# Kernel tuning notes

Measured on AMD Instinct MI355X. Metric: run time of the kernel, lower is better.

Reference implementation:

```python
import jax, jax.numpy as jnp
import numpy as np

EPS_KERAS = 1e-7  # keras backend epsilon used by SparseCategoricalCrossentropy clipping


def _box_terms(p_boxes, g_boxes):
    # boxes are cxcywh; module uses pixel-style '+1' widths. Returns (iou, bg_ratio).
    p_ul = p_boxes[..., :2] - 0.5 * p_boxes[..., 2:]
    p_dr = p_boxes[..., :2] + 0.5 * p_boxes[..., 2:]
    g_ul = g_boxes[..., :2] - 0.5 * g_boxes[..., 2:]
    g_dr = g_boxes[..., :2] + 0.5 * g_boxes[..., 2:]
    inter_wh = jnp.maximum(jnp.minimum(p_dr, g_dr) - jnp.maximum(p_ul, g_ul) + 1.0, 0.0)
    inter = inter_wh[..., 0] * inter_wh[..., 1]
    p_wh = jnp.maximum(p_dr - p_ul + 1.0, 0.0)
    g_wh = jnp.maximum(g_dr - g_ul + 1.0, 0.0)
    p_area = p_wh[..., 0] * p_wh[..., 1]
    g_area = g_wh[..., 0] * g_wh[..., 1]
    union = p_area + g_area - inter
    iou = inter / jnp.maximum(union, 1e-9)
    bound_wh = jnp.maximum(jnp.maximum(p_dr, g_dr) - jnp.minimum(p_ul, g_ul) + 1.0, 0.0)
    bound = bound_wh[..., 0] * bound_wh[..., 1]
    bg_ratio = (bound - union) / jnp.maximum(bound, 1e-9)
    return iou, bg_ratio


def _cost_matrix(bbox_pred, labels_pred, bbox_gt, labels_gt):
    # Vectorized over batch: [B,Q,G] pairwise L1 + (-GIoU) + (-prob of gt class)
    bp = bbox_pred[:, :, None, :]   # [B,Q,1,4]
    bg = bbox_gt[:, None, :, :]     # [B,1,G,4]
    l1 = jnp.sum(jnp.abs(bp - bg), axis=-1)
    iou, bg_ratio = _box_terms(bp, bg)
    B, Q, _ = labels_pred.shape
    G = labels_gt.shape[1]
    idx = jnp.broadcast_to(labels_gt[:, None, :].astype(jnp.int32), (B, Q, G))
    probs = jnp.take_along_axis(labels_pred, idx, axis=2)
    return l1 - (iou - bg_ratio) - probs


def _hungarian(cost):
    # Exact min-cost assignment for a square matrix (Jonker-Volgenant style,
    # e-maxx Hungarian). Host-side, mirrors scipy.optimize.linear_sum_assignment.
    cost = np.asarray(cost, dtype=np.float64)
    n = cost.shape[0]
    u = np.zeros(n + 1)
    v = np.zeros(n + 1)
    p = np.zeros(n + 1, dtype=np.int64)    # p[j]: row matched to column j (1-based)
    way = np.zeros(n + 1, dtype=np.int64)
    for i in range(1, n + 1):
        p[0] = i
        j0 = 0
        minv = np.full(n + 1, np.inf)
        used = np.zeros(n + 1, dtype=bool)
        while True:
            used[j0] = True
            i0 = p[j0]
            cur = cost[i0 - 1] - u[i0] - v[1:]
            free = ~used[1:]
            better = free & (cur < minv[1:])
            minv[1:][better] = cur[better]
            way[1:][better] = j0
            masked = np.where(free, minv[1:], np.inf)
            j1 = int(np.argmin(masked)) + 1
            delta = masked[j1 - 1]
            uidx = np.nonzero(used)[0]
            u[p[uidx]] += delta
            v[uidx] -= delta
            minv[~used] -= delta
            j0 = j1
            if p[j0] == 0:
                break
        while j0 != 0:
            j1 = way[j0]
            p[j0] = p[j1]
            j0 = j1
    ans = np.zeros(n, dtype=np.int64)
    ans[p[1:] - 1] = np.arange(n)   # ans[row] = matched col
    return ans


def _losses(bbox_pred, labels_pred, bbox_gt, labels_gt, col):
    # col: [B,Q] matched gt column per query (row_ind is arange for square cost).
    # Label loss: scatter of matched gt labels onto queries == gather by col,
    # then keras SparseCategoricalCrossentropy(from_logits=False):
    # clip probs to [eps,1-eps], log, softmax-CE (== -log p for normalized probs).
    query_labels = jnp.take_along_axis(labels_gt.astype(jnp.int32), col, axis=1)  # [B,Q]
    logits = jnp.log(jnp.clip(labels_pred, EPS_KERAS, 1.0 - EPS_KERAS))
    logp = jax.nn.log_softmax(logits, axis=-1)
    nll = -jnp.take_along_axis(logp, query_labels[..., None], axis=-1)[..., 0]    # [B,Q]
    label_loss = jnp.mean(nll, axis=1)
    # Bbox L1: pred rows gathered by arange (identity), gt gathered by col.
    target = jnp.take_along_axis(bbox_gt, col[..., None], axis=1)                 # [B,Q,4]
    reg_loss = jnp.mean(jnp.abs(bbox_pred - target), axis=(1, 2))
    # GIoU term: original code uses UN-permuted gt here (faithful to source),
    # and adds +mean(iou - bg_ratio) (sign as in source).
    iou, bg_ratio = _box_terms(bbox_pred, bbox_gt)
    giou = jnp.mean(iou - bg_ratio, axis=1)
    per_sample = 1.0 * label_loss + 5.0 * reg_loss + 2.0 * giou
    return jnp.sum(per_sample)


def reference(bbox_pred, labels_pred, bbox_gt, labels_gt):
    cost = np.asarray(_cost_matrix(bbox_pred, labels_pred, bbox_gt, labels_gt))
    col = jnp.asarray(np.stack([_hungarian(c) for c in cost]))  # [B,Q]
    return _losses(bbox_pred, labels_pred, bbox_gt, labels_gt, col)


def setup_inputs() -> dict:
    key = jax.random.key(0)
    k1, k2, k3, k4 = jax.random.split(key, 4)
    B, Q, G, C = 16, 100, 100, 100
    bbox_pred = jax.random.uniform(k1, (B, Q, 4), dtype=jnp.float32)
    labels_pred = jax.nn.softmax(jax.random.normal(k2, (B, Q, C), dtype=jnp.float32), axis=-1)
    bbox_gt = jax.random.uniform(k3, (B, G, 4), dtype=jnp.float32)
    labels_gt = jax.random.randint(k4, (B, G), 0, C, dtype=jnp.int32)
    return {"bbox_pred": bbox_pred, "labels_pred": labels_pred, "bbox_gt": bbox_gt, "labels_gt": labels_gt}
```

## Files before the change

### kernel.cpp

```cpp
#include <hip/hip_runtime.h>
#include <math.h>

#define NB 100

__device__ __forceinline__ void box_terms(const float bp[4], const float bg[4],
                                          float &iou, float &bgr) {
    float p_ul0 = bp[0] - 0.5f * bp[2], p_ul1 = bp[1] - 0.5f * bp[3];
    float p_dr0 = bp[0] + 0.5f * bp[2], p_dr1 = bp[1] + 0.5f * bp[3];
    float g_ul0 = bg[0] - 0.5f * bg[2], g_ul1 = bg[1] - 0.5f * bg[3];
    float g_dr0 = bg[0] + 0.5f * bg[2], g_dr1 = bg[1] + 0.5f * bg[3];
    float iw0 = fmaxf(fminf(p_dr0, g_dr0) - fmaxf(p_ul0, g_ul0) + 1.0f, 0.0f);
    float iw1 = fmaxf(fminf(p_dr1, g_dr1) - fmaxf(p_ul1, g_ul1) + 1.0f, 0.0f);
    float inter = iw0 * iw1;
    float pw0 = fmaxf(p_dr0 - p_ul0 + 1.0f, 0.0f);
    float pw1 = fmaxf(p_dr1 - p_ul1 + 1.0f, 0.0f);
    float gw0 = fmaxf(g_dr0 - g_ul0 + 1.0f, 0.0f);
    float gw1 = fmaxf(g_dr1 - g_ul1 + 1.0f, 0.0f);
    float pa = pw0 * pw1, ga = gw0 * gw1;
    float uni = pa + ga - inter;
    iou = inter / fmaxf(uni, 1e-9f);
    float bw0 = fmaxf(fmaxf(p_dr0, g_dr0) - fminf(p_ul0, g_ul0) + 1.0f, 0.0f);
    float bw1 = fmaxf(fmaxf(p_dr1, g_dr1) - fminf(p_ul1, g_ul1) + 1.0f, 0.0f);
    float bound = bw0 * bw1;
    bgr = (bound - uni) / fmaxf(bound, 1e-9f);
}

template<int CTRL>
__device__ __forceinline__ double dpp_f64(double x) {
    int lo = __builtin_amdgcn_update_dpp(0, __double2loint(x), CTRL, 0xF, 0xF, true);
    int hi = __builtin_amdgcn_update_dpp(0, __double2hiint(x), CTRL, 0xF, 0xF, true);
    return __hiloint2double(hi, lo);
}

template<int CTRL>
__device__ __forceinline__ double dpp_f64_keep(double x) {
    int lo = __builtin_amdgcn_update_dpp(__double2loint(x), __double2loint(x),
                                         CTRL, 0xF, 0xF, false);
    int hi = __builtin_amdgcn_update_dpp(__double2hiint(x), __double2hiint(x),
                                         CTRL, 0xF, 0xF, false);
    return __hiloint2double(hi, lo);
}

__device__ __forceinline__ double readlane_f64(double x, int l) {
    int lo = __builtin_amdgcn_readlane(__double2loint(x), l);
    int hi = __builtin_amdgcn_readlane(__double2hiint(x), l);
    return __hiloint2double(hi, lo);
}

__device__ __forceinline__ double wave_min_f64(double x) {
    double q1 = dpp_f64<0xB1>(x);
    double q2 = dpp_f64<0x4E>(x);
    double q3 = dpp_f64<0x1B>(x);
    x = fmin(fmin(x, q1), fmin(q2, q3));
    double h1 = dpp_f64<0x141>(x);
    double h2 = dpp_f64<0x140>(x);
    double h3 = dpp_f64_keep<0x118>(x);
    x = fmin(fmin(x, h1), fmin(h2, h3));
    x = fmin(x, dpp_f64<0x142>(x));
    x = fmin(x, dpp_f64<0x143>(x));
    return readlane_f64(x, 63);
}

__device__ __forceinline__ double wave_min_packed(double x, int &lo_out) {
    double q1 = dpp_f64<0xB1>(x);
    double q2 = dpp_f64<0x4E>(x);
    double q3 = dpp_f64<0x1B>(x);
    x = fmin(fmin(x, q1), fmin(q2, q3));
    double h1 = dpp_f64<0x141>(x);
    double h2 = dpp_f64<0x140>(x);
    double h3 = dpp_f64_keep<0x118>(x);
    x = fmin(fmin(x, h1), fmin(h2, h3));
    x = fmin(x, dpp_f64<0x142>(x));
    x = fmin(x, dpp_f64<0x143>(x));
    int lo = __builtin_amdgcn_readlane(__double2loint(x), 63);
    int hi = __builtin_amdgcn_readlane(__double2hiint(x), 63);
    lo_out = lo;
    return __hiloint2double(hi, lo);
}

__device__ __forceinline__ double pack_tag(double g, int tag) {
    unsigned long long bi = (unsigned long long)__double_as_longlong(g);
    bi = (bi & ~0x3FFFULL) | (unsigned long long)(unsigned)tag;
    return __longlong_as_double((long long)bi);
}

__global__ __launch_bounds__(256) void fused_match_loss(
    const float* __restrict__ bbox_pred,
    const float* __restrict__ labels_pred,
    const float* __restrict__ bbox_gt,
    const int*   __restrict__ labels_gt,
    float* __restrict__ out)
{
    __shared__ float  cost_sh[NB * NB + 64];
    __shared__ double u_sh[NB];
    __shared__ double v_sh[NB];
    __shared__ int    rowclaim_sh[NB];
    __shared__ int    col_sh[NB];
    __shared__ float  bp_sh[NB * 4];
    __shared__ float  bg_sh[NB * 4];
    __shared__ int    lg_sh[NB];
    __shared__ float  red_sh[3 * 128];

    const int b = blockIdx.x;
    const int t = threadIdx.x;
    const int lane = t & 63;
    const bool hasB = (lane + 64 < NB);
    const double INF = (double)INFINITY;
    const double QNAN = __longlong_as_double(0x7FF8000000000000LL);
    const float* lp = labels_pred + (size_t)b * NB * NB;

    double vA = 0.0, vB = 0.0;
    double uA = 0.0, uB = 0.0;
    int pA = -1, pB = -1;
    unsigned long long remLo = 0, remHi = 0;

    for (int i = t; i < NB * 4; i += 256) {
        bp_sh[i] = bbox_pred[(size_t)b * NB * 4 + i];
        bg_sh[i] = bbox_gt[(size_t)b * NB * 4 + i];
    }
    for (int i = t; i < NB; i += 256) {
        lg_sh[i] = labels_gt[b * NB + i];
        rowclaim_sh[i] = 0x7FFFFFFF;
    }
    __syncthreads();

    for (int idx = t; idx < NB * NB; idx += 256) {
        int q = idx / NB, g = idx - q * NB;
        float bp[4] = {bp_sh[q*4+0], bp_sh[q*4+1], bp_sh[q*4+2], bp_sh[q*4+3]};
        float bg[4] = {bg_sh[g*4+0], bg_sh[g*4+1], bg_sh[g*4+2], bg_sh[g*4+3]};
        float l1 = fabsf(bp[0]-bg[0]) + fabsf(bp[1]-bg[1])
                 + fabsf(bp[2]-bg[2]) + fabsf(bp[3]-bg[3]);
        float iou, bgr;
        box_terms(bp, bg, iou, bgr);
        float prob = lp[q * NB + lg_sh[g]];
        cost_sh[idx] = l1 - (iou - bgr) - prob;
    }
    __syncthreads();

    if (t < 64) {
        float bestA = INFINITY, bestB = INFINITY;
        int iminA = 0, iminB = 0;
        for (int i = 0; i < NB; ++i) {
            float cA = cost_sh[i * NB + lane];
            float cB = cost_sh[i * NB + lane + 64];
            if (cA < bestA) { bestA = cA; iminA = i; }
            if (hasB && cB < bestB) { bestB = cB; iminB = i; }
        }
        atomicMin(&rowclaim_sh[iminA], lane);
        if (hasB) atomicMin(&rowclaim_sh[iminB], lane + 64);

        vA = (double)bestA;
        vB = hasB ? (double)bestB : 0.0;
        v_sh[lane] = vA;
        if (hasB) v_sh[lane + 64] = vB;
        pA = (rowclaim_sh[iminA] == lane) ? iminA : -1;
        pB = (hasB && rowclaim_sh[iminB] == lane + 64) ? iminB : -1;
        remLo = __ballot(rowclaim_sh[lane] == 0x7FFFFFFF);
        remHi = __ballot(hasB && rowclaim_sh[lane + 64] == 0x7FFFFFFF);
    }
    __syncthreads();

    {
        const int w = t >> 6;
        for (int i = w; i < NB; i += 4) {
            double r = (double)cost_sh[i * NB + lane] - v_sh[lane];
            if (hasB)
                r = fmin(r, (double)cost_sh[i * NB + lane + 64] - v_sh[lane + 64]);
            r = wave_min_f64(r);
            if (lane == 0)
                u_sh[i] = (rowclaim_sh[i] != 0x7FFFFFFF) ? 0.0 : r;
        }
    }
    __syncthreads();

    if (t < 64) {
        {
            unsigned long long gLo = remLo, gHi = remHi;
            while (gLo | gHi) {
                int i;
                if (gLo) { i = __ffsll((long long)gLo) - 1; gLo &= gLo - 1; }
                else { i = 64 + __ffsll((long long)gHi) - 1; gHi &= gHi - 1; }
                double u_i = u_sh[i];
                const float* crow = &cost_sh[i * NB];
                double rdA = (double)crow[lane] - u_i - vA;
                double rdB = (double)crow[lane + 64] - u_i - vB;
                unsigned long long ba = __ballot(pA < 0 && rdA == 0.0);
                unsigned long long bb = __ballot(hasB && pB < 0 && rdB == 0.0);
                if (ba) {
                    int wl = __ffsll((long long)ba) - 1;
                    if (lane == wl) { pA = i; uA = u_i; }
                } else if (bb) {
                    int wl = __ffsll((long long)bb) - 1;
                    if (lane == wl) { pB = i; uB = u_i; }
                } else continue;
                if (i < 64) remLo &= ~(1ull << i); else remHi &= ~(1ull << (i - 64));
            }
        }

        auto phase = [&](int irow) {
            double GAq = QNAN, GBq = QNAN;
            int wayA = -1, wayB = -1;
            bool usedA = false, usedB = !hasB;
            double DusedA = 0.0, DusedB = 0.0;
            double D = 0.0;
            int jprevmark = -1;
            double u0 = u_sh[irow];
            double Df; int jfin;

            const int tagA = ((pA + 1) << 7) | lane;
            const int tagB = ((pB + 1) << 7) | (lane + 64);

            float cA = cost_sh[irow * NB + lane];
            float cB = cost_sh[irow * NB + lane + 64];

            for (;;) {
                double du = D - u0;
                double candAq = pack_tag(((double)cA - vA) + du, tagA);
                if (!usedA && !(candAq >= GAq)) { GAq = candAq; wayA = jprevmark; }
                double candBq = pack_tag(((double)cB - vB) + du, tagB);
                if (!usedB && !(candBq >= GBq)) { GBq = candBq; wayB = jprevmark; }
                int wlo;
                const double m = wave_min_packed(fmin(GAq, GBq), wlo);
                const int j1 = wlo & 0x7F;
                const int prow = ((wlo >> 7) & 0x7F) - 1;
                const bool isA = (j1 < 64);
                const int winLane = j1 & 63;
                if (prow < 0) { Df = m; jfin = j1; break; }
                cA = cost_sh[prow * NB + lane];
                cB = cost_sh[prow * NB + lane + 64];
                double unext = readlane_f64(isA ? uA : uB, winLane);
                if (lane == winLane) {
                    if (isA) { usedA = true; DusedA = m; GAq = QNAN; }
                    else     { usedB = true; DusedB = m; GBq = QNAN; }
                }
                u0 = unext; jprevmark = j1; D = m;
            }

            if (usedA) { uA += Df - DusedA; vA -= Df - DusedA; }
            if (hasB && usedB) { uB += Df - DusedB; vB -= Df - DusedB; }

            int jcur = jfin;
            while (jcur != -1) {
                int wl = jcur & 63;
                int jprev = (jcur < 64) ? __builtin_amdgcn_readlane(wayA, wl)
                                        : __builtin_amdgcn_readlane(wayB, wl);
                int row; double unew;
                if (jprev < 0) { row = irow; unew = u_sh[irow] + Df; }
                else {
                    int pl = jprev & 63;
                    int rA = __builtin_amdgcn_readlane(pA, pl);
                    int rB = __builtin_amdgcn_readlane(pB, pl);
                    double xA = readlane_f64(uA, pl);
                    double xB = readlane_f64(uB, pl);
                    row  = (jprev < 64) ? rA : rB;
                    unew = (jprev < 64) ? xA : xB;
                }
                if (jcur < 64) { if (lane == jcur)      { pA = row; uA = unew; } }
                else           { if (lane == jcur - 64) { pB = row; uB = unew; } }
                jcur = jprev;
            }
        };

        while (remLo) { int i = __ffsll((long long)remLo) - 1; remLo &= remLo - 1; phase(i); }
        while (remHi) { int i = 64 + __ffsll((long long)remHi) - 1; remHi &= remHi - 1; phase(i); }

        if (pA >= 0) col_sh[pA] = lane;
        if (hasB && pB >= 0) col_sh[pB] = lane + 64;
    }
    __syncthreads();

    float nll = 0.0f, regsum = 0.0f, giou = 0.0f;
    if (t < NB) {
        const int q = t;
        const int cg = col_sh[q];
        const int cidx = lg_sh[cg];
        const float* row = lp + q * NB;
        const float hi = 1.0f - 1e-7f;
        float mx = -INFINITY;
        for (int k = 0; k < NB; ++k) {
            float lg = logf(fminf(fmaxf(row[k], 1e-7f), hi));
            mx = fmaxf(mx, lg);
        }
        float se = 0.0f, logit_c = 0.0f;
        for (int k = 0; k < NB; ++k) {
            float lg = logf(fminf(fmaxf(row[k], 1e-7f), hi));
            se += expf(lg - mx);
            if (k == cidx) logit_c = lg;
        }
        nll = (mx + logf(se)) - logit_c;

        for (int k = 0; k < 4; ++k)
            regsum += fabsf(bp_sh[q*4+k] - bg_sh[cg*4+k]);

        float bp[4] = {bp_sh[q*4+0], bp_sh[q*4+1], bp_sh[q*4+2], bp_sh[q*4+3]};
        float bq[4] = {bg_sh[q*4+0], bg_sh[q*4+1], bg_sh[q*4+2], bg_sh[q*4+3]};
        float iou, bgr;
        box_terms(bp, bq, iou, bgr);
        giou = iou - bgr;
    }
    if (t < 128) {
        red_sh[t]       = nll;
        red_sh[128 + t] = regsum;
        red_sh[256 + t] = giou;
    }
    __syncthreads();
    if (t < 64) {
        float a = red_sh[t]       + red_sh[t + 64];
        float r = red_sh[128 + t] + red_sh[128 + t + 64];
        float g = red_sh[256 + t] + red_sh[256 + t + 64];
        #pragma unroll
        for (int off = 32; off > 0; off >>= 1) {
            a += __shfl_xor(a, off, 64);
            r += __shfl_xor(r, off, 64);
            g += __shfl_xor(g, off, 64);
        }
        if (t == 0) {
            float ps = a * (1.0f / NB) + 5.0f * (r * (1.0f / (NB * 4)))
                     + 2.0f * (g * (1.0f / NB));
            atomicAdd(out, ps);
        }
    }
}

extern "C" void kernel_launch(void* const* d_in, const int* in_sizes, int n_in,
                              void* d_out, int out_size, void* d_ws, size_t ws_size,
                              hipStream_t stream) {
    const float* bbox_pred   = (const float*)d_in[0];
    const float* labels_pred = (const float*)d_in[1];
    const float* bbox_gt     = (const float*)d_in[2];
    const int*   labels_gt   = (const int*)d_in[3];
    float* out = (float*)d_out;

    const int B = in_sizes[0] / (NB * 4);

    fused_match_loss<<<B, 256, 0, stream>>>(bbox_pred, labels_pred, bbox_gt,
                                            labels_gt, out);
}
```

Measured before the change: 366.5 us.

## Add augmenting row reduction passes before Hungarian shortest-path phase

Inserts two passes of Jonker-Volgenant augmenting row reduction. For each still-unassigned row, the pass finds the two smallest reduced costs using wave-wide packed minimum reductions, then assigns the row and adjusts the column duals. A displaced row continues within the same pass when the minimum is strict and is otherwise re-queued. The aim is to assign most rows cheaply so that fewer rows need the costlier shortest-augmenting-path phase. A cap on the number of scans bounds the extra work, and the risk is that the added scans outweigh the savings when few rows get resolved.

```diff
diff --git a/kernel.cpp b/kernel.cpp
--- a/kernel.cpp
+++ b/kernel.cpp
@@ -197,6 +197,72 @@
             }
         }
 
+        {
+            int scans = 0;
+            bool bail = false;
+            for (int pass = 0; pass < 2 && !bail; ++pass) {
+                unsigned long long curLo = remLo, curHi = remHi;
+                remLo = 0; remHi = 0;
+                int i = -1;
+                float cAr = 0.0f, cBr = 0.0f;
+                for (;;) {
+                    if (i < 0) {
+                        if (curLo)      { i = __ffsll((long long)curLo) - 1; curLo &= curLo - 1; }
+                        else if (curHi) { i = 64 + __ffsll((long long)curHi) - 1; curHi &= curHi - 1; }
+                        else break;
+                        cAr = cost_sh[i * NB + lane];
+                        cBr = cost_sh[i * NB + lane + 64];
+                    }
+                    if (++scans > 1200) {
+                        if (i < 64) remLo |= 1ull << i; else remHi |= 1ull << (i - 64);
+                        remLo |= curLo; remHi |= curHi;
+                        bail = true; break;
+                    }
+                    double candA = pack_tag((double)cAr - vA, ((pA + 1) << 7) | lane);
+                    double candB = hasB ? pack_tag((double)cBr - vB,
+                                                   ((pB + 1) << 7) | (lane + 64))
+                                        : QNAN;
+                    int wlo1;
+                    double m1 = wave_min_packed(fmin(candA, candB), wlo1);
+                    int j1 = wlo1 & 0x7F;
+                    int i0 = ((wlo1 >> 7) & 0x7F) - 1;
+                    float sA = 0.0f, sB = 0.0f;
+                    if (i0 >= 0) {
+                        sA = cost_sh[i0 * NB + lane];
+                        sB = cost_sh[i0 * NB + lane + 64];
+                    }
+                    double eA = (lane == j1)        ? QNAN : candA;
+                    double eB = (lane + 64 == j1)   ? QNAN : candB;
+                    int wlo2;
+                    double m2 = wave_min_packed(fmin(eA, eB), wlo2);
+                    bool strict = (m1 < m2);
+                    if (!strict && i0 >= 0) {
+                        j1 = wlo2 & 0x7F;
+                        i0 = ((wlo2 >> 7) & 0x7F) - 1;
+                    }
+                    const int wl = j1 & 63;
+                    const bool isA = (j1 < 64);
+                    if (i0 >= 0) {
+                        double oldu = readlane_f64(isA ? uA : uB, wl);
+                        if (lane == 0) u_sh[i0] = oldu;
+                    }
+                    if (lane == wl) {
+                        if (isA) { if (strict) vA -= (m2 - m1); pA = i; uA = m2; }
+                        else     { if (strict) vB -= (m2 - m1); pB = i; uB = m2; }
+                    }
+                    if (i0 >= 0 && strict) {
+                        i = i0; cAr = sA; cBr = sB;
+                    } else {
+                        if (i0 >= 0) {
+                            if (i0 < 64) remLo |= 1ull << i0;
+                            else         remHi |= 1ull << (i0 - 64);
+                        }
+                        i = -1;
+                    }
+                }
+            }
+        }
+
         auto phase = [&](int irow) {
             double GAq = QNAN, GBq = QNAN;
             int wayA = -1, wayB = -1;
```

Result: slower. 857.2 us (+133.9%).

## Add augmenting row-reduction pass and parallel u init for free rows

Applied to the files above, without the earlier changes.

After the greedy column-reduction matching, a Jonker-Volgenant style reduction transfer adjusts v for each already assigned row using its second-smallest reduced cost. All four waves then initialize u for the unassigned rows in parallel from the updated v. The aim is tighter dual variables so the serial shortest-augmenting-path phases, run by a single wave, need fewer iterations. The cost is an extra serial pass with a wave reduction per assigned row plus two block barriers.

```diff
diff --git a/kernel.cpp b/kernel.cpp
--- a/kernel.cpp
+++ b/kernel.cpp
@@ -96,6 +96,7 @@
     __shared__ double v_sh[NB];
     __shared__ int    rowclaim_sh[NB];
     __shared__ int    col_sh[NB];
+    __shared__ unsigned long long remmask_sh[2];
     __shared__ float  bp_sh[NB * 4];
     __shared__ float  bg_sh[NB * 4];
     __shared__ int    lg_sh[NB];
@@ -105,7 +106,6 @@
     const int t = threadIdx.x;
     const int lane = t & 63;
     const bool hasB = (lane + 64 < NB);
-    const double INF = (double)INFINITY;
     const double QNAN = __longlong_as_double(0x7FF8000000000000LL);
     const float* lp = labels_pred + (size_t)b * NB * NB;
 
@@ -197,6 +197,60 @@
             }
         }
 
+        {
+            unsigned long long aLo = ~remLo;
+            unsigned long long aHi = (~remHi) & ((1ull << (NB - 64)) - 1);
+            while (aLo | aHi) {
+                int i;
+                if (aLo) { i = __ffsll((long long)aLo) - 1; aLo &= aLo - 1; }
+                else { i = 64 + __ffsll((long long)aHi) - 1; aHi &= aHi - 1; }
+                unsigned long long mA = __ballot(pA == i);
+                unsigned long long mB = __ballot(hasB && pB == i);
+                if (!(mA | mB)) continue;
+                const int j1 = mA ? (__ffsll((long long)mA) - 1)
+                                  : 64 + (__ffsll((long long)mB) - 1);
+                float cAr = cost_sh[i * NB + lane];
+                float cBr = cost_sh[i * NB + lane + 64];
+                double rA2 = (lane == j1) ? QNAN : (double)cAr - vA;
+                double rB2 = (!hasB || lane + 64 == j1) ? QNAN
+                                                        : (double)cBr - vB;
+                double min2_ = wave_min_f64(fmin(rA2, rB2));
+                const int wl = j1 & 63;
+                if (lane == wl) {
+                    if (j1 < 64) {
+                        double dlt = min2_ - uA;
+                        if (dlt > 0.0) { vA -= dlt; uA = min2_; }
+                    } else {
+                        double dlt = min2_ - uB;
+                        if (dlt > 0.0) { vB -= dlt; uB = min2_; }
+                    }
+                }
+            }
+        }
+
+        v_sh[lane] = vA;
+        if (hasB) v_sh[lane + 64] = vB;
+        if (lane == 0) { remmask_sh[0] = remLo; remmask_sh[1] = remHi; }
+    }
+    __syncthreads();
+
+    {
+        const int w = t >> 6;
+        for (int i = w; i < NB; i += 4) {
+            const bool isfree = (i < 64)
+                ? ((remmask_sh[0] >> i) & 1ull)
+                : ((remmask_sh[1] >> (i - 64)) & 1ull);
+            if (!isfree) continue;
+            double r = (double)cost_sh[i * NB + lane] - v_sh[lane];
+            if (hasB)
+                r = fmin(r, (double)cost_sh[i * NB + lane + 64] - v_sh[lane + 64]);
+            r = wave_min_f64(r);
+            if (lane == 0) u_sh[i] = r;
+        }
+    }
+    __syncthreads();
+
+    if (t < 64) {
         auto phase = [&](int irow) {
             double GAq = QNAN, GBq = QNAN;
             int wayA = -1, wayB = -1;
```

Result: slower. 382.3 us (+4.3%).

## Use multi-source Dijkstra augmentation from all unmatched rows in Hungarian phases

Applied to the files above, without the earlier changes.

Replaces the per-row augmenting-path phase with a multi-source shortest-path search seeded from every remaining unassigned row at once. A software-pipelined prefetch of cost rows and duals initializes the minimum slack per column along with its source row, and each phase augments along whichever source yields the cheapest path. The goal is shorter Dijkstra searches and fewer serial wave-min iterations, at the cost of an initialization pass over all remaining rows each phase. A fallback drops one row when no source wins, which could alter exact assignment semantics in edge cases.

```diff
diff --git a/kernel.cpp b/kernel.cpp
--- a/kernel.cpp
+++ b/kernel.cpp
@@ -105,7 +105,6 @@
     const int t = threadIdx.x;
     const int lane = t & 63;
     const bool hasB = (lane + 64 < NB);
-    const double INF = (double)INFINITY;
     const double QNAN = __longlong_as_double(0x7FF8000000000000LL);
     const float* lp = labels_pred + (size_t)b * NB * NB;
 
@@ -197,28 +196,53 @@
             }
         }
 
-        auto phase = [&](int irow) {
+        auto phase_ms = [&]() -> int {
             double GAq = QNAN, GBq = QNAN;
             int wayA = -1, wayB = -1;
+            int srcA = 0,  srcB = 0;
             bool usedA = false, usedB = !hasB;
             double DusedA = 0.0, DusedB = 0.0;
-            double D = 0.0;
-            int jprevmark = -1;
-            double u0 = u_sh[irow];
             double Df; int jfin;
 
             const int tagA = ((pA + 1) << 7) | lane;
             const int tagB = ((pB + 1) << 7) | (lane + 64);
 
-            float cA = cost_sh[irow * NB + lane];
-            float cB = cost_sh[irow * NB + lane + 64];
+            {
+                unsigned long long mLo = remLo, mHi = remHi;
+                int i0 = -1, i1 = -1, i2 = -1;
+                float a0 = 0, b0 = 0, a1 = 0, b1 = 0, a2 = 0, b2 = 0;
+                double u0 = 0, u1 = 0, u2 = 0;
+                #define FETCH_ROW(ii, aa, bb, uu)                              \
+                    do {                                                       \
+                        if (mLo) { ii = __ffsll((long long)mLo) - 1;           \
+                                   mLo &= mLo - 1; }                           \
+                        else if (mHi) { ii = 64 + __ffsll((long long)mHi) - 1; \
+                                        mHi &= mHi - 1; }                      \
+                        else ii = -1;                                          \
+                        if (ii >= 0) {                                         \
+                            aa = cost_sh[ii * NB + lane];                      \
+                            bb = cost_sh[ii * NB + lane + 64];                 \
+                            uu = u_sh[ii];                                     \
+                        }                                                      \
+                    } while (0)
+                FETCH_ROW(i0, a0, b0, u0);
+                FETCH_ROW(i1, a1, b1, u1);
+                FETCH_ROW(i2, a2, b2, u2);
+                while (i0 >= 0) {
+                    double candA = pack_tag((double)a0 - vA - u0, tagA);
+                    if (!(candA >= GAq)) { GAq = candA; wayA = -1; srcA = i0; }
+                    if (hasB) {
+                        double candB = pack_tag((double)b0 - vB - u0, tagB);
+                        if (!(candB >= GBq)) { GBq = candB; wayB = -1; srcB = i0; }
+                    }
+                    i0 = i1; a0 = a1; b0 = b1; u0 = u1;
+                    i1 = i2; a1 = a2; b1 = b2; u1 = u2;
+                    FETCH_ROW(i2, a2, b2, u2);
+                }
+                #undef FETCH_ROW
+            }
 
             for (;;) {
-                double du = D - u0;
-                double candAq = pack_tag(((double)cA - vA) + du, tagA);
-                if (!usedA && !(candAq >= GAq)) { GAq = candAq; wayA = jprevmark; }
-                double candBq = pack_tag(((double)cB - vB) + du, tagB);
-                if (!usedB && !(candBq >= GBq)) { GBq = candBq; wayB = jprevmark; }
                 int wlo;
                 const double m = wave_min_packed(fmin(GAq, GBq), wlo);
                 const int j1 = wlo & 0x7F;
@@ -226,27 +250,36 @@
                 const bool isA = (j1 < 64);
                 const int winLane = j1 & 63;
                 if (prow < 0) { Df = m; jfin = j1; break; }
-                cA = cost_sh[prow * NB + lane];
-                cB = cost_sh[prow * NB + lane + 64];
+                float cA = cost_sh[prow * NB + lane];
+                float cB = cost_sh[prow * NB + lane + 64];
                 double unext = readlane_f64(isA ? uA : uB, winLane);
                 if (lane == winLane) {
                     if (isA) { usedA = true; DusedA = m; GAq = QNAN; }
                     else     { usedB = true; DusedB = m; GBq = QNAN; }
                 }
-                u0 = unext; jprevmark = j1; D = m;
+                double du = m - unext;
+                double candAq = pack_tag(((double)cA - vA) + du, tagA);
+                if (!usedA && !(candAq >= GAq)) { GAq = candAq; wayA = j1; }
+                double candBq = pack_tag(((double)cB - vB) + du, tagB);
+                if (!usedB && !(candBq >= GBq)) { GBq = candBq; wayB = j1; }
             }
 
             if (usedA) { uA += Df - DusedA; vA -= Df - DusedA; }
             if (hasB && usedB) { uB += Df - DusedB; vB -= Df - DusedB; }
 
             int jcur = jfin;
+            int iwin = -1;
             while (jcur != -1) {
                 int wl = jcur & 63;
                 int jprev = (jcur < 64) ? __builtin_amdgcn_readlane(wayA, wl)
                                         : __builtin_amdgcn_readlane(wayB, wl);
                 int row; double unew;
-                if (jprev < 0) { row = irow; unew = u_sh[irow] + Df; }
-                else {
+                if (jprev < 0) {
+                    row = (jcur < 64) ? __builtin_amdgcn_readlane(srcA, wl)
+                                      : __builtin_amdgcn_readlane(srcB, wl);
+                    unew = u_sh[row] + Df;
+                    iwin = row;
+                } else {
                     int pl = jprev & 63;
                     int rA = __builtin_amdgcn_readlane(pA, pl);
                     int rB = __builtin_amdgcn_readlane(pB, pl);
@@ -259,10 +292,21 @@
                 else           { if (lane == jcur - 64) { pB = row; uB = unew; } }
                 jcur = jprev;
             }
+            return iwin;
         };
 
-        while (remLo) { int i = __ffsll((long long)remLo) - 1; remLo &= remLo - 1; phase(i); }
-        while (remHi) { int i = 64 + __ffsll((long long)remHi) - 1; remHi &= remHi - 1; phase(i); }
+        while (remLo | remHi) {
+            int iwin = phase_ms();
+            unsigned long long nLo = remLo, nHi = remHi;
+            if (iwin >= 0) {
+                if (iwin < 64) nLo &= ~(1ull << iwin);
+                else           nHi &= ~(1ull << (iwin - 64));
+            }
+            if (nLo == remLo && nHi == remHi) {
+                if (nLo) nLo &= nLo - 1; else nHi &= nHi - 1;
+            }
+            remLo = nLo; remHi = nHi;
+        }
 
         if (pA >= 0) col_sh[pA] = lane;
         if (hasB && pB >= 0) col_sh[pB] = lane + 64;
```

Measured after the change: 545.8 us. 1.49x slower.
